# Kernel optimization log

Hardware: AMD Instinct MI355X
Metric: run time of the kernel (lower is better)

## Reference

```python
import jax, jax.numpy as jnp
import numpy as np

BITW = 1
BITA = 3
BATCH = 8192
IN_CH = 4096
N_UNITS = 4096


def _quantize(x, k):
    # DoReFa uniform quantizer with straight-through estimator (round -> identity grad)
    n = float(2 ** k - 1)
    return x + jax.lax.stop_gradient(jnp.round(x * n) / n - x)


def _cabs(x):
    # clip magnitude to [0, 1]
    return jnp.minimum(1.0, jnp.abs(x))


def quantize_active(x, bitA):
    if bitA == 32:
        return x
    return _quantize(x, bitA)


def quantize_weight(w, bitW):
    if bitW == 32:
        return w
    if bitW == 1:
        # binary weights scaled by mean |w| (E is treated as constant)
        E = jax.lax.stop_gradient(jnp.mean(jnp.abs(w)))
        y = w / E
        # sign with straight-through gradient
        return (y + jax.lax.stop_gradient(jnp.sign(y) - y)) * E
    t = jnp.tanh(w)
    t = t / jnp.max(jnp.abs(t)) * 0.5 + 0.5
    return 2.0 * _quantize(t, bitW) - 1.0


def setup_inputs() -> dict:
    key = jax.random.key(0)
    k1, k2 = jax.random.split(key)
    inputs = jax.random.normal(k1, (BATCH, IN_CH), dtype=jnp.float32)
    # truncated_normal(stddev=0.1) init approximated with normal * 0.1
    W = jax.random.normal(k2, (IN_CH, N_UNITS), dtype=jnp.float32) * 0.1
    b = jnp.zeros((N_UNITS,), dtype=jnp.float32)
    return {"inputs": inputs, "W": W, "b": b}


def reference(inputs, W, b):
    q_in = quantize_active(_cabs(inputs), BITA)   # [B, IN] in {0..1} grid of 2^bitA-1 levels
    q_W = quantize_weight(W, BITW)                # [IN, OUT] binary (+-E)
    out = jnp.matmul(q_in, q_W) + b               # [B, OUT]
    return out
```

## Files before the change

kernel.cpp:

```cpp
#include <hip/hip_runtime.h>


static constexpr int BATCH  = 8192;
static constexpr int IN_CH  = 4096;
static constexpr int NUNITS = 4096;
static constexpr int TPB    = 256;

typedef int v4i __attribute__((ext_vector_type(4)));

static constexpr size_t A8_OFF   = 0;
static constexpr size_t A8_BYTES = (size_t)BATCH * IN_CH;
static constexpr size_t BT_OFF   = A8_OFF + A8_BYTES;
static constexpr size_t BT_BYTES = (size_t)NUNITS * IN_CH;
static constexpr int    NPART    = 4096;
static constexpr size_t PART_OFF = BT_OFF + BT_BYTES;
static constexpr size_t SCALE_OFF= PART_OFF + NPART * sizeof(float);

__global__ __launch_bounds__(TPB) void k_signT(const float* __restrict__ W,
                                               char* __restrict__ bt,
                                               float* __restrict__ partials) {
    __shared__ char tile[64][68];
    __shared__ float red[TPB];
    const int bk = blockIdx.x & 63;
    const int bn = blockIdx.x >> 6;
    const int t  = threadIdx.x;
    const int c  = t & 63;
    const int r0 = t >> 6;
    float asum = 0.f;
#pragma unroll
    for (int i = 0; i < 16; ++i) {
        int r = i * 4 + r0;
        float w = W[(size_t)(bk * 64 + r) * NUNITS + bn * 64 + c];
        asum += fabsf(w);
        tile[c][r] = (w > 0.f) ? 1 : ((w < 0.f) ? -1 : 0);
    }
    __syncthreads();
    const int n  = t >> 2;
    const int kk = (t & 3) * 16;
    char o[16];
#pragma unroll
    for (int j = 0; j < 16; ++j) o[j] = tile[n][kk + j];
    *(uint4*)(bt + (size_t)(bn * 64 + n) * IN_CH + bk * 64 + kk) = *(const uint4*)o;

    red[t] = asum;
    __syncthreads();
    for (int off = TPB / 2; off > 0; off >>= 1) {
        if (t < off) red[t] += red[t + off];
        __syncthreads();
    }
    if (t == 0) partials[blockIdx.x] = red[0];
}

__device__ __forceinline__ unsigned int q4(float4 v) {
    unsigned int b0 = (unsigned int)(int)rintf(fminf(1.0f, fabsf(v.x)) * 7.0f);
    unsigned int b1 = (unsigned int)(int)rintf(fminf(1.0f, fabsf(v.y)) * 7.0f);
    unsigned int b2 = (unsigned int)(int)rintf(fminf(1.0f, fabsf(v.z)) * 7.0f);
    unsigned int b3 = (unsigned int)(int)rintf(fminf(1.0f, fabsf(v.w)) * 7.0f);
    return b0 | (b1 << 8) | (b2 << 16) | (b3 << 24);
}

__global__ __launch_bounds__(TPB) void k_quant_a(const float4* __restrict__ x4,
                                                 uint4* __restrict__ a16,
                                                 const float* __restrict__ partials,
                                                 float* __restrict__ scale) {
    if (blockIdx.x == 0) {
        __shared__ float red[TPB];
        float s = 0.f;
        for (int i = threadIdx.x; i < NPART; i += TPB) s += partials[i];
        red[threadIdx.x] = s;
        __syncthreads();
        for (int off = TPB / 2; off > 0; off >>= 1) {
            if ((int)threadIdx.x < off) red[threadIdx.x] += red[threadIdx.x + off];
            __syncthreads();
        }
        if (threadIdx.x == 0) {
            float E = red[0] / (float)((size_t)IN_CH * NUNITS);
            *scale = E / 7.0f;
        }
    }
    const size_t t = (size_t)blockIdx.x * TPB + threadIdx.x;
    uint4 o;
    o.x = q4(x4[t * 4 + 0]);
    o.y = q4(x4[t * 4 + 1]);
    o.z = q4(x4[t * 4 + 2]);
    o.w = q4(x4[t * 4 + 3]);
    a16[t] = o;
}

__device__ __forceinline__ void gload_lds16(const void* g, void* l) {
    __builtin_amdgcn_global_load_lds((const __attribute__((address_space(1))) void*)g,
                                     (__attribute__((address_space(3))) void*)l,
                                     16, 0, 0);
}

#define VMCNT2   asm volatile("s_waitcnt vmcnt(2)" ::: "memory")
#define VMCNT0   asm volatile("s_waitcnt vmcnt(0)" ::: "memory")
#define LGKM0    asm volatile("s_waitcnt lgkmcnt(0)" ::: "memory")
#define SCHEDB   __builtin_amdgcn_sched_barrier(0)
#define BARRIER  __builtin_amdgcn_s_barrier()
#define PRIO1    __builtin_amdgcn_s_setprio(1)
#define PRIO0    __builtin_amdgcn_s_setprio(0)

static constexpr int NT = IN_CH / 64;

__global__ __launch_bounds__(1024, 4) void k_gemm(const char* __restrict__ A8,
                                                  const char* __restrict__ BT,
                                                  const float* __restrict__ scale_p,
                                                  const float* __restrict__ bias,
                                                  float* __restrict__ out) {
    __shared__ char Ms[3][32768];

    const int t    = threadIdx.x;
    const int bid  = blockIdx.x;
    const int swzb = (bid & 7) * 64 + (bid >> 3);
    const int bRow = swzb >> 4;
    const int bCol = swzb & 15;
    const int lane = t & 63;
    const int wid  = t >> 6;
    const int wr   = wid >> 2;
    const int wc   = wid & 3;
    const int lr   = lane & 15;
    const int lk4  = lane >> 4;

    const int aoff = ((lk4 ^ (lr & 7)) << 4);
    const int boff = aoff ^ 64;

    const int lslot = (t & 7) ^ ((t >> 3) & 7);
    const char* mbase = (lslot < 4)
        ? (A8 + (size_t)(bRow * 256) * IN_CH)
        : (BT + (size_t)(bCol * 256) * IN_CH);
    const char* sbase = mbase + (size_t)(t >> 3) * IN_CH + ((lslot & 3) << 4);

    v4i acc[4][4] = {};

#define STAGE2(kt, STG)                                                          \
    _Pragma("unroll") for (int h = 0; h < 2; ++h)                                \
        gload_lds16(sbase + (size_t)h * 128 * IN_CH + (size_t)(kt) * 64,         \
                    (STG) + h * 16384 + t * 16)

#define TILE(kt, CUR, STG, LAST)                                                 \
    do {                                                                         \
        SCHEDB; LGKM0;                                                           \
        if (LAST) { VMCNT0; } else { VMCNT2; }                                   \
        BARRIER; SCHEDB;                                                         \
        if ((kt) + 2 < NT) { STAGE2((kt) + 2, STG); }                            \
        v4i a_[4], b_[4];                                                        \
        _Pragma("unroll") for (int m = 0; m < 4; ++m)                            \
            a_[m] = *(const v4i*)((CUR) + (wr * 64 + m * 16 + lr) * 128 + aoff); \
        _Pragma("unroll") for (int n = 0; n < 4; ++n)                            \
            b_[n] = *(const v4i*)((CUR) + (wc * 64 + n * 16 + lr) * 128 + boff); \
        PRIO1;                                                                   \
        _Pragma("unroll") for (int m = 0; m < 4; ++m)                            \
            _Pragma("unroll") for (int n = 0; n < 4; ++n)                        \
                acc[m][n] = __builtin_amdgcn_mfma_i32_16x16x64_i8(               \
                    a_[m], b_[n], acc[m][n], 0, 0, 0);                           \
        PRIO0;                                                                   \
    } while (0)

    char* B0 = (char*)Ms[0];
    char* B1 = (char*)Ms[1];
    char* B2 = (char*)Ms[2];

    STAGE2(0, B0);
    STAGE2(1, B1);

    for (int T = 0; T < NT - 1; T += 3) {
        TILE(T,     B0, B2, false);
        TILE(T + 1, B1, B0, false);
        TILE(T + 2, B2, B1, false);
    }
    TILE(NT - 1, B0, B2, true);

    const float scale = *scale_p;
    const int orow0 = bRow * 256 + wr * 64;
    const int ocol0 = bCol * 256 + wc * 64;
#pragma unroll
    for (int m = 0; m < 4; ++m) {
#pragma unroll
        for (int n = 0; n < 4; ++n) {
            const int col = ocol0 + n * 16 + lr;
            const float bb = bias[col];
            const int rbase = orow0 + m * 16 + lk4 * 4;
#pragma unroll
            for (int j = 0; j < 4; ++j)
                out[(size_t)(rbase + j) * NUNITS + col] = scale * (float)acc[m][n][j] + bb;
        }
    }
#undef STAGE2
#undef TILE
}

extern "C" void kernel_launch(void* const* d_in, const int* in_sizes, int n_in,
                              void* d_out, int out_size, void* d_ws, size_t ws_size,
                              hipStream_t stream) {
    const float* x  = (const float*)d_in[0];
    const float* W  = (const float*)d_in[1];
    const float* b  = (const float*)d_in[2];
    float* out      = (float*)d_out;

    char*  ws       = (char*)d_ws;
    char*  A8       = ws + A8_OFF;
    char*  BT       = ws + BT_OFF;
    float* partials = (float*)(ws + PART_OFF);
    float* scale    = (float*)(ws + SCALE_OFF);

    k_signT<<<(IN_CH / 64) * (NUNITS / 64), TPB, 0, stream>>>(W, BT, partials);
    k_quant_a<<<(BATCH * (IN_CH / 16)) / TPB, TPB, 0, stream>>>((const float4*)x, (uint4*)A8,
                                                                partials, scale);
    k_gemm<<<(BATCH / 256) * (NUNITS / 256), 1024, 0, stream>>>(A8, BT, scale, b, out);
}
```

Measured before the change: 173.4 us.

## Pre-swizzle activations into MFMA fragment layout and load A directly from global

The activation quantizer now writes the int8 activations in a fragment-ordered layout so each GEMM lane can read its 16-byte MFMA A operand straight from global memory. The GEMM stops staging A through LDS, halving shared memory per stage and issuing one async LDS load per tile (B only) with adjusted waitcnt. This removes the LDS round-trip and bank traffic for A but makes the A loads synchronous global reads in the inner loop, which rely on cache hits and may expose latency.

```diff
diff --git a/kernel.cpp b/kernel.cpp
--- a/kernel.cpp
+++ b/kernel.cpp
@@ -8,9 +8,9 @@
 
 typedef int v4i __attribute__((ext_vector_type(4)));
 
-static constexpr size_t A8_OFF   = 0;
-static constexpr size_t A8_BYTES = (size_t)BATCH * IN_CH;
-static constexpr size_t BT_OFF   = A8_OFF + A8_BYTES;
+static constexpr size_t AF_OFF   = 0;
+static constexpr size_t AF_BYTES = (size_t)BATCH * IN_CH;
+static constexpr size_t BT_OFF   = AF_OFF + AF_BYTES;
 static constexpr size_t BT_BYTES = (size_t)NUNITS * IN_CH;
 static constexpr int    NPART    = 4096;
 static constexpr size_t PART_OFF = BT_OFF + BT_BYTES;
@@ -59,8 +59,8 @@
     return b0 | (b1 << 8) | (b2 << 16) | (b3 << 24);
 }
 
-__global__ __launch_bounds__(TPB) void k_quant_a(const float4* __restrict__ x4,
-                                                 uint4* __restrict__ a16,
+__global__ __launch_bounds__(TPB) void k_quant_a(const float* __restrict__ x,
+                                                 char* __restrict__ af,
                                                  const float* __restrict__ partials,
                                                  float* __restrict__ scale) {
     if (blockIdx.x == 0) {
@@ -77,14 +77,23 @@
             float E = red[0] / (float)((size_t)IN_CH * NUNITS);
             *scale = E / 7.0f;
         }
-    }
-    const size_t t = (size_t)blockIdx.x * TPB + threadIdx.x;
-    uint4 o;
-    o.x = q4(x4[t * 4 + 0]);
-    o.y = q4(x4[t * 4 + 1]);
-    o.z = q4(x4[t * 4 + 2]);
-    o.w = q4(x4[t * 4 + 3]);
-    a16[t] = o;
+        __syncthreads();
+    }
+    __shared__ uint4 lds[64][5];
+    const int t  = threadIdx.x;
+    const int br = blockIdx.x >> 6;
+    const int bc = blockIdx.x & 63;
+    const int r  = t >> 2;
+    const int cs = t & 3;
+    const float4* xp = (const float4*)x + ((size_t)(br * 64 + r) * 1024 + bc * 16 + cs * 4);
+    uint4 q;
+    q.x = q4(xp[0]); q.y = q4(xp[1]); q.z = q4(xp[2]); q.w = q4(xp[3]);
+    lds[r][cs] = q;
+    __syncthreads();
+    const int m    = t >> 6;
+    const int lane = t & 63;
+    uint4 o = lds[m * 16 + (lane & 15)][lane >> 4];
+    *(uint4*)(af + ((((size_t)(br * 4 + m)) * 64 + bc) << 10) + lane * 16) = o;
 }
 
 __device__ __forceinline__ void gload_lds16(const void* g, void* l) {
@@ -93,7 +102,7 @@
                                      16, 0, 0);
 }
 
-#define VMCNT2   asm volatile("s_waitcnt vmcnt(2)" ::: "memory")
+#define VMCNT1   asm volatile("s_waitcnt vmcnt(1)" ::: "memory")
 #define VMCNT0   asm volatile("s_waitcnt vmcnt(0)" ::: "memory")
 #define LGKM0    asm volatile("s_waitcnt lgkmcnt(0)" ::: "memory")
 #define SCHEDB   __builtin_amdgcn_sched_barrier(0)
@@ -103,12 +112,12 @@
 
 static constexpr int NT = IN_CH / 64;
 
-__global__ __launch_bounds__(1024, 4) void k_gemm(const char* __restrict__ A8,
+__global__ __launch_bounds__(1024, 4) void k_gemm(const char* __restrict__ AF,
                                                   const char* __restrict__ BT,
                                                   const float* __restrict__ scale_p,
                                                   const float* __restrict__ bias,
                                                   float* __restrict__ out) {
-    __shared__ char Ms[3][32768];
+    __shared__ char Bs[3][16384];
 
     const int t    = threadIdx.x;
     const int bid  = blockIdx.x;
@@ -122,33 +131,36 @@
     const int lr   = lane & 15;
     const int lk4  = lane >> 4;
 
-    const int aoff = ((lk4 ^ (lr & 7)) << 4);
-    const int boff = aoff ^ 64;
-
-    const int lslot = (t & 7) ^ ((t >> 3) & 7);
-    const char* mbase = (lslot < 4)
-        ? (A8 + (size_t)(bRow * 256) * IN_CH)
-        : (BT + (size_t)(bCol * 256) * IN_CH);
-    const char* sbase = mbase + (size_t)(t >> 3) * IN_CH + ((lslot & 3) << 4);
+    const char* aBaseF = AF + (((size_t)(bRow * 16 + wr * 4) * 64) << 10) + lane * 16;
+
+    int boff[4];
+#pragma unroll
+    for (int n = 0; n < 4; ++n) {
+        const int R    = wc * 64 + n * 16 + lr;
+        const int line = R & 127;
+        const int phys = (((R >> 7) << 2) | lk4) ^ (line & 7);
+        boff[n] = line * 128 + phys * 16;
+    }
+
+    const int x_    = (t & 7) ^ ((t >> 3) & 7);
+    const int srow  = (t >> 3) + ((x_ >> 2) << 7);
+    const char* sB  = BT + (size_t)(bCol * 256 + srow) * IN_CH + ((x_ & 3) << 4);
 
     v4i acc[4][4] = {};
 
-#define STAGE2(kt, STG)                                                          \
-    _Pragma("unroll") for (int h = 0; h < 2; ++h)                                \
-        gload_lds16(sbase + (size_t)h * 128 * IN_CH + (size_t)(kt) * 64,         \
-                    (STG) + h * 16384 + t * 16)
-
-#define TILE(kt, CUR, STG, LAST)                                                 \
+#define STAGE1(kt, STG)  gload_lds16(sB + (size_t)(kt) * 64, (STG) + t * 16)
+
+#define TILE(kt, CUR, STG, GATE)                                                 \
     do {                                                                         \
         SCHEDB; LGKM0;                                                           \
-        if (LAST) { VMCNT0; } else { VMCNT2; }                                   \
+        GATE;                                                                    \
         BARRIER; SCHEDB;                                                         \
-        if ((kt) + 2 < NT) { STAGE2((kt) + 2, STG); }                            \
+        if ((kt) + 2 < NT) { STAGE1((kt) + 2, STG); }                            \
         v4i a_[4], b_[4];                                                        \
         _Pragma("unroll") for (int m = 0; m < 4; ++m)                            \
-            a_[m] = *(const v4i*)((CUR) + (wr * 64 + m * 16 + lr) * 128 + aoff); \
+            a_[m] = *(const v4i*)(aBaseF + (((size_t)m * 64 + (kt)) << 10));     \
         _Pragma("unroll") for (int n = 0; n < 4; ++n)                            \
-            b_[n] = *(const v4i*)((CUR) + (wc * 64 + n * 16 + lr) * 128 + boff); \
+            b_[n] = *(const v4i*)((CUR) + boff[n]);                              \
         PRIO1;                                                                   \
         _Pragma("unroll") for (int m = 0; m < 4; ++m)                            \
             _Pragma("unroll") for (int n = 0; n < 4; ++n)                        \
@@ -157,19 +169,19 @@
         PRIO0;                                                                   \
     } while (0)
 
-    char* B0 = (char*)Ms[0];
-    char* B1 = (char*)Ms[1];
-    char* B2 = (char*)Ms[2];
-
-    STAGE2(0, B0);
-    STAGE2(1, B1);
+    char* B0 = (char*)Bs[0];
+    char* B1 = (char*)Bs[1];
+    char* B2 = (char*)Bs[2];
+
+    STAGE1(0, B0);
+    STAGE1(1, B1);
 
     for (int T = 0; T < NT - 1; T += 3) {
-        TILE(T,     B0, B2, false);
-        TILE(T + 1, B1, B0, false);
-        TILE(T + 2, B2, B1, false);
-    }
-    TILE(NT - 1, B0, B2, true);
+        TILE(T,     B0, B2, VMCNT1);
+        TILE(T + 1, B1, B0, VMCNT1);
+        TILE(T + 2, B2, B1, VMCNT1);
+    }
+    TILE(NT - 1, B0, B2, VMCNT0);
 
     const float scale = *scale_p;
     const int orow0 = bRow * 256 + wr * 64;
@@ -186,7 +198,7 @@
                 out[(size_t)(rbase + j) * NUNITS + col] = scale * (float)acc[m][n][j] + bb;
         }
     }
-#undef STAGE2
+#undef STAGE1
 #undef TILE
 }
 
@@ -199,13 +211,12 @@
     float* out      = (float*)d_out;
 
     char*  ws       = (char*)d_ws;
-    char*  A8       = ws + A8_OFF;
+    char*  AF       = ws + AF_OFF;
     char*  BT       = ws + BT_OFF;
     float* partials = (float*)(ws + PART_OFF);
     float* scale    = (float*)(ws + SCALE_OFF);
 
     k_signT<<<(IN_CH / 64) * (NUNITS / 64), TPB, 0, stream>>>(W, BT, partials);
-    k_quant_a<<<(BATCH * (IN_CH / 16)) / TPB, TPB, 0, stream>>>((const float4*)x, (uint4*)A8,
-                                                                partials, scale);
-    k_gemm<<<(BATCH / 256) * (NUNITS / 256), 1024, 0, stream>>>(A8, BT, scale, b, out);
-}
+    k_quant_a<<<(BATCH / 64) * (IN_CH / 64), TPB, 0, stream>>>(x, AF, partials, scale);
+    k_gemm<<<(BATCH / 256) * (NUNITS / 256), 1024, 0, stream>>>(AF, BT, scale, b, out);
+}
```

Measured after the change: 219.4 us. 1.27x slower.

## Switch GEMM from triple-buffered 64-K tiles to double-buffered 128-K intervals

Applied to the files above, without the earlier changes.

The int8 GEMM main loop moves from a three-stage ring of 64-wide K tiles (prefetch distance two, waiting with vmcnt(2)) to two 64KB buffers each holding 128 K values. Each interval waits for all outstanding loads, issues the next interval's loads, then runs two 64-K MFMA chunks. This halves the number of barriers per K step, at the cost of a shallower prefetch depth (one interval ahead) and a full vmcnt(0) drain at each barrier.

```diff
diff --git a/kernel.cpp b/kernel.cpp
--- a/kernel.cpp
+++ b/kernel.cpp
@@ -93,7 +93,6 @@
                                      16, 0, 0);
 }
 
-#define VMCNT2   asm volatile("s_waitcnt vmcnt(2)" ::: "memory")
 #define VMCNT0   asm volatile("s_waitcnt vmcnt(0)" ::: "memory")
 #define LGKM0    asm volatile("s_waitcnt lgkmcnt(0)" ::: "memory")
 #define SCHEDB   __builtin_amdgcn_sched_barrier(0)
@@ -101,14 +100,14 @@
 #define PRIO1    __builtin_amdgcn_s_setprio(1)
 #define PRIO0    __builtin_amdgcn_s_setprio(0)
 
-static constexpr int NT = IN_CH / 64;
+static constexpr int NI = IN_CH / 128;
 
 __global__ __launch_bounds__(1024, 4) void k_gemm(const char* __restrict__ A8,
                                                   const char* __restrict__ BT,
                                                   const float* __restrict__ scale_p,
                                                   const float* __restrict__ bias,
                                                   float* __restrict__ out) {
-    __shared__ char Ms[3][32768];
+    __shared__ char Ms[2][65536];
 
     const int t    = threadIdx.x;
     const int bid  = blockIdx.x;
@@ -133,22 +132,20 @@
 
     v4i acc[4][4] = {};
 
-#define STAGE2(kt, STG)                                                          \
-    _Pragma("unroll") for (int h = 0; h < 2; ++h)                                \
-        gload_lds16(sbase + (size_t)h * 128 * IN_CH + (size_t)(kt) * 64,         \
-                    (STG) + h * 16384 + t * 16)
-
-#define TILE(kt, CUR, STG, LAST)                                                 \
+#define STAGE4(P, STG)                                                           \
+    _Pragma("unroll") for (int c = 0; c < 2; ++c)                                \
+        _Pragma("unroll") for (int h = 0; h < 2; ++h)                            \
+            gload_lds16(sbase + (size_t)h * 128 * IN_CH + ((size_t)(P) * 128 + c * 64), \
+                        (STG) + c * 32768 + h * 16384 + t * 16)
+
+#define CHUNK(CUR, c)                                                            \
     do {                                                                         \
-        SCHEDB; LGKM0;                                                           \
-        if (LAST) { VMCNT0; } else { VMCNT2; }                                   \
-        BARRIER; SCHEDB;                                                         \
-        if ((kt) + 2 < NT) { STAGE2((kt) + 2, STG); }                            \
+        const char* _cp = (CUR) + (c) * 32768;                                   \
         v4i a_[4], b_[4];                                                        \
         _Pragma("unroll") for (int m = 0; m < 4; ++m)                            \
-            a_[m] = *(const v4i*)((CUR) + (wr * 64 + m * 16 + lr) * 128 + aoff); \
+            a_[m] = *(const v4i*)(_cp + (wr * 64 + m * 16 + lr) * 128 + aoff);   \
         _Pragma("unroll") for (int n = 0; n < 4; ++n)                            \
-            b_[n] = *(const v4i*)((CUR) + (wc * 64 + n * 16 + lr) * 128 + boff); \
+            b_[n] = *(const v4i*)(_cp + (wc * 64 + n * 16 + lr) * 128 + boff);   \
         PRIO1;                                                                   \
         _Pragma("unroll") for (int m = 0; m < 4; ++m)                            \
             _Pragma("unroll") for (int n = 0; n < 4; ++n)                        \
@@ -157,19 +154,27 @@
         PRIO0;                                                                   \
     } while (0)
 
+#define INTERVAL(P, CUR, STG, DOSTG)                                             \
+    do {                                                                         \
+        SCHEDB; LGKM0;                                                           \
+        VMCNT0;                                                                  \
+        BARRIER; SCHEDB;                                                         \
+        if (DOSTG) { STAGE4((P) + 1, STG); }                                     \
+        CHUNK(CUR, 0);                                                           \
+        CHUNK(CUR, 1);                                                           \
+    } while (0)
+
     char* B0 = (char*)Ms[0];
     char* B1 = (char*)Ms[1];
-    char* B2 = (char*)Ms[2];
-
-    STAGE2(0, B0);
-    STAGE2(1, B1);
-
-    for (int T = 0; T < NT - 1; T += 3) {
-        TILE(T,     B0, B2, false);
-        TILE(T + 1, B1, B0, false);
-        TILE(T + 2, B2, B1, false);
-    }
-    TILE(NT - 1, B0, B2, true);
+
+    STAGE4(0, B0);
+
+    for (int P = 0; P < NI - 2; P += 2) {
+        INTERVAL(P,     B0, B1, 1);
+        INTERVAL(P + 1, B1, B0, 1);
+    }
+    INTERVAL(NI - 2, B0, B1, 1);
+    INTERVAL(NI - 1, B1, B0, 0);
 
     const float scale = *scale_p;
     const int orow0 = bRow * 256 + wr * 64;
@@ -186,8 +191,9 @@
                 out[(size_t)(rbase + j) * NUNITS + col] = scale * (float)acc[m][n][j] + bb;
         }
     }
-#undef STAGE2
-#undef TILE
+#undef STAGE4
+#undef CHUNK
+#undef INTERVAL
 }
 
 extern "C" void kernel_launch(void* const* d_in, const int* in_sizes, int n_in,
```

Result: faster. 166.9 us (-3.8%).
